# Optimization experiments

Hardware: AMD Instinct MI355X
Metric: run time of the kernel (lower is better)

The kernel has to match this reference:

```python
import jax, jax.numpy as jnp
import numpy as np

B, N, IN_DIM, ATT_DIM = 2, 8192, 512, 512


def setup_inputs() -> dict:
    key = jax.random.key(0)
    k1, k2, k3, k4 = jax.random.split(key, 4)
    X = jax.random.normal(k1, (B, N, IN_DIM), dtype=jnp.float32)
    adj = jax.random.uniform(k2, (B, N, N), dtype=jnp.float32)
    mask = jnp.ones((B, N), dtype=jnp.float32)
    # Learned params (torch Linear stores W as (out,in); we store (in,out) for x @ W)
    Wqk = jax.random.normal(k3, (IN_DIM, 2 * ATT_DIM), dtype=jnp.float32) / np.sqrt(IN_DIM)
    Wv = jax.random.normal(k4, (IN_DIM, IN_DIM), dtype=jnp.float32) / np.sqrt(IN_DIM)
    return {"X": X, "adj": adj, "mask": mask, "Wqk": Wqk, "Wv": Wv}


def reference(X, adj, mask, Wqk, Wv):
    # q, k: (B, N, att_dim); v: (B, N, in_dim)
    qk = X @ Wqk
    q, k = jnp.split(qk, 2, axis=-1)
    v = X @ Wv
    att_dim = q.shape[-1]
    inv_scale = 1.0 / jnp.sqrt(jnp.float32(att_dim))
    # Original math: w_i = inv_scale * sum_j adj_ij * m_i * m_j * (q_i . k_j).
    # Since the rank-1 mask factors (m_i m_j), fold m_j into k and m_i into the row
    # score, avoiding a second materialized NxN tensor:
    k_m = k * mask[:, :, None]                       # (B, N, att_dim)
    agg = jnp.einsum("bij,bjd->bid", adj, k_m)       # (B, N, att_dim)
    w = inv_scale * mask * jnp.einsum("bid,bid->bi", q, agg)  # (B, N)
    # softmax over the bag dimension (dim=1), then scale v rows
    L = jax.nn.softmax(w, axis=1)[:, :, None] * v    # (B, N, in_dim)
    return L
```

## Files before the change

### kernel.cpp

```cpp
#include <hip/hip_runtime.h>
#include <math.h>

#define BB 2
#define NN 8192
#define DD 512

static const float INV_SCALE = 0.04419417382415922f;

typedef short s16x8 __attribute__((ext_vector_type(8)));
typedef unsigned short u16x8 __attribute__((ext_vector_type(8)));
typedef float f32x4 __attribute__((ext_vector_type(4)));

#define AS1 __attribute__((address_space(1)))
#define AS3 __attribute__((address_space(3)))

__device__ __forceinline__ unsigned short bfbits(__bf16 h) {
    return __builtin_bit_cast(unsigned short, h);
}

__device__ __forceinline__ void gll16(const void* g, void* l) {
    __builtin_amdgcn_global_load_lds((const AS1 unsigned int*)g, (AS3 unsigned int*)l, 16, 0, 0);
}

__global__ __launch_bounds__(256) void convx_k(
    const float* __restrict__ X, unsigned short* __restrict__ Xhi,
    unsigned short* __restrict__ Xlo)
{
    long i = (long)blockIdx.x * 256 + threadIdx.x;
    float4 x = ((const float4*)X)[i];
    __bf16 h0 = (__bf16)x.x, h1 = (__bf16)x.y, h2 = (__bf16)x.z, h3 = (__bf16)x.w;
    ushort4 hi4 = make_ushort4(bfbits(h0), bfbits(h1), bfbits(h2), bfbits(h3));
    __bf16 l0 = (__bf16)(x.x - (float)h0), l1 = (__bf16)(x.y - (float)h1);
    __bf16 l2 = (__bf16)(x.z - (float)h2), l3 = (__bf16)(x.w - (float)h3);
    ushort4 lo4 = make_ushort4(bfbits(l0), bfbits(l1), bfbits(l2), bfbits(l3));
    ((ushort4*)Xhi)[i] = hi4;
    ((ushort4*)Xlo)[i] = lo4;
}

__global__ __launch_bounds__(256) void convw_k(
    const float* __restrict__ Wqk, const float* __restrict__ Wv,
    unsigned short* __restrict__ QTh, unsigned short* __restrict__ QTl,
    unsigned short* __restrict__ VTh, unsigned short* __restrict__ VTl)
{
    int i = blockIdx.x * 256 + threadIdx.x;
    float val; unsigned short *ph, *pl;
    if (i < 524288) {
        int n = i >> 9, k = i & 511;
        val = Wqk[k * 1024 + n]; ph = QTh + i; pl = QTl + i;
    } else {
        int o = i - 524288; int n = o >> 9, k = o & 511;
        val = Wv[k * 512 + n]; ph = VTh + o; pl = VTl + o;
    }
    __bf16 h = (__bf16)val;
    __bf16 l = (__bf16)(val - (float)h);
    *ph = bfbits(h); *pl = bfbits(l);
}

template <int EPI, int NT>
__global__ __launch_bounds__(256, 2) void mfma_gemm(
    const unsigned short* __restrict__ A0, const unsigned short* __restrict__ A1,
    const unsigned short* __restrict__ B0, const unsigned short* __restrict__ B1,
    float* __restrict__ C,
    float* __restrict__ q, float* __restrict__ km,
    unsigned short* __restrict__ kmT, const float* __restrict__ mask,
    int N, int K)
{
    constexpr int BK = 32;
    constexpr int TILE_SH = 128 * BK;

    __shared__ unsigned short Asm[2 * TILE_SH];
    __shared__ unsigned short Bsm[2 * TILE_SH];

    const int t = threadIdx.x;
    const int wv = t >> 6, lane = t & 63;
    const int wm = wv >> 1, wn = wv & 1;
    const long m0 = blockIdx.x * 128;
    const int n0 = blockIdx.y * 128;

    f32x4 acc[4][4];
#pragma unroll
    for (int i = 0; i < 4; ++i)
#pragma unroll
        for (int j = 0; j < 4; ++j) acc[i][j] = {0.f, 0.f, 0.f, 0.f};

    const int swzcol = ((lane & 3) ^ ((lane >> 2) & 3)) * 16;
    auto stageA16 = [&](int term, int k0, int buf) {
        const unsigned short* Ab = (term < 2) ? A0 : A1;
#pragma unroll
        for (int u = 0; u < 2; ++u) {
            int c = wv * 2 + u;
            int row = c * 16 + (lane >> 2);
            gll16((const char*)Ab + ((m0 + row) * (long)K + k0) * 2 + swzcol,
                  (char*)Asm + buf * (TILE_SH * 2) + c * 1024);
        }
    };
    auto stageB16 = [&](int term, int k0, int buf) {
        const unsigned short* Bb = (NT == 3 && term == 1) ? B1 : B0;
#pragma unroll
        for (int u = 0; u < 2; ++u) {
            int c = wv * 2 + u;
            int row = c * 16 + (lane >> 2);
            gll16((const char*)Bb + ((long)(n0 + row) * K + k0) * 2 + swzcol,
                  (char*)Bsm + buf * (TILE_SH * 2) + c * 1024);
        }
    };

    stageA16(0, 0, 0);
    stageB16(0, 0, 0);
    __syncthreads();

    const int NTILES = NT * (K / BK);
    int cur = 0, term = 0, k0 = 0;
    const int g = lane >> 4;

#pragma unroll 2
    for (int tt = 0; tt < NTILES; ++tt) {
        int k0n = k0 + BK, termn = term;
        if (k0n == K) { k0n = 0; ++termn; }
        const bool hasNext = (tt + 1 < NTILES);

        if (hasNext) {
            stageA16(termn, k0n, cur ^ 1);
            stageB16(termn, k0n, cur ^ 1);
        }

        s16x8 av[4], bv[4];
#pragma unroll
        for (int f = 0; f < 4; ++f) {
            int ra = wm * 64 + f * 16 + (lane & 15);
            int rb = wn * 64 + f * 16 + (lane & 15);
            av[f] = *(const s16x8*)(Asm + cur * TILE_SH + ra * BK + ((g ^ (ra & 3)) << 3));
            bv[f] = *(const s16x8*)(Bsm + cur * TILE_SH + rb * BK + ((g ^ (rb & 3)) << 3));
        }
#pragma unroll
        for (int fm = 0; fm < 4; ++fm)
#pragma unroll
            for (int fn = 0; fn < 4; ++fn)
                acc[fm][fn] = __builtin_amdgcn_mfma_f32_16x16x32_bf16(
                    av[fm], bv[fn], acc[fm][fn], 0, 0, 0);

        __syncthreads();
        cur ^= 1; term = termn; k0 = k0n;
    }

    const long rbase = m0 + wm * 64;
    const int cbase = n0 + wn * 64;

    if constexpr (EPI == 0) {
#pragma unroll
        for (int fm = 0; fm < 4; ++fm) {
            long rb = rbase + fm * 16 + ((lane >> 4) << 2);
#pragma unroll
            for (int fn = 0; fn < 4; ++fn) {
                int c = cbase + fn * 16 + (lane & 15);
#pragma unroll
                for (int j = 0; j < 4; ++j)
                    C[(rb + j) * (long)N + c] = acc[fm][fn][j];
            }
        }
    } else {
        const bool isq = (n0 < 512);
#pragma unroll
        for (int fm = 0; fm < 4; ++fm) {
            long rb = rbase + fm * 16 + ((lane >> 4) << 2);
#pragma unroll
            for (int fn = 0; fn < 4; ++fn) {
                int c = cbase + fn * 16 + (lane & 15);
                if (isq) {
#pragma unroll
                    for (int j = 0; j < 4; ++j)
                        q[(rb + j) * 512L + c] = acc[fm][fn][j];
                } else {
                    int c2 = c - 512;
                    float kv[4];
#pragma unroll
                    for (int j = 0; j < 4; ++j) {
                        kv[j] = acc[fm][fn][j] * mask[rb + j];
                        km[(rb + j) * 512L + c2] = kv[j];
                    }
                    ushort4 pk = make_ushort4(bfbits((__bf16)kv[0]), bfbits((__bf16)kv[1]),
                                              bfbits((__bf16)kv[2]), bfbits((__bf16)kv[3]));
                    long b = rb >> 13, r = rb & 8191;
                    *(ushort4*)(kmT + (b << 22) + ((long)c2 << 13) + r) = pk;
                }
            }
        }
    }
}

__global__ __launch_bounds__(256, 2) void adj_gemm(
    const float* __restrict__ adj,
    const unsigned short* __restrict__ kmT,
    const float* __restrict__ q,
    float* __restrict__ w)
{
    constexpr int BK = 64;
    constexpr int TS = 128 * BK;
    constexpr int NT = NN / BK;

    __shared__ unsigned short Asm[2 * TS];
    __shared__ unsigned short Bsm[2 * TS];

    const int t = threadIdx.x;
    const int wv = t >> 6, lane = t & 63;
    const int wm = wv >> 1, wn = wv & 1;
    const int z = blockIdx.z;
    const long m0 = blockIdx.x * 128;
    const int n0 = blockIdx.y * 128;

    const float* Az = adj + (long)z * NN * NN;
    const unsigned short* Bz = kmT + ((long)z << 22);

    f32x4 acc[4][4];
#pragma unroll
    for (int i = 0; i < 4; ++i)
#pragma unroll
        for (int j = 0; j < 4; ++j) acc[i][j] = {0.f, 0.f, 0.f, 0.f};

    const int bswz = ((lane & 7) ^ (lane >> 3)) << 4;
    auto stageB = [&](int ttile, int buf) {
        const int k0 = ttile * BK;
#pragma unroll
        for (int u = 0; u < 4; ++u) {
            int c = wv * 4 + u;
            int row = c * 8 + (lane >> 3);
            gll16((const char*)Bz + ((long)(n0 + row) * NN + k0) * 2 + bswz,
                  (char*)Bsm + buf * (TS * 2) + c * 1024);
        }
    };

    const int arow = t >> 1;
    const int asl0 = (t & 1) * 4;
    auto issueA = [&](int ttile, float4 (&r)[8]) {
        const float* s = Az + (m0 + arow) * (long)NN + ttile * BK + asl0 * 8;
#pragma unroll
        for (int u = 0; u < 4; ++u) {
            r[2 * u]     = *(const float4*)(s + u * 8);
            r[2 * u + 1] = *(const float4*)(s + u * 8 + 4);
        }
    };
    auto commitA = [&](float4 (&r)[8], int buf) {
#pragma unroll
        for (int u = 0; u < 4; ++u) {
            float4 a = r[2 * u], b = r[2 * u + 1];
            u16x8 pk;
            pk[0] = bfbits((__bf16)a.x); pk[1] = bfbits((__bf16)a.y);
            pk[2] = bfbits((__bf16)a.z); pk[3] = bfbits((__bf16)a.w);
            pk[4] = bfbits((__bf16)b.x); pk[5] = bfbits((__bf16)b.y);
            pk[6] = bfbits((__bf16)b.z); pk[7] = bfbits((__bf16)b.w);
            *(u16x8*)(Asm + buf * TS + arow * 64 + (((asl0 + u) ^ (arow & 7)) << 3)) = pk;
        }
    };

    const int g = lane >> 4;
    auto compute = [&](int buf) {
#pragma unroll
        for (int ks = 0; ks < 2; ++ks) {
            s16x8 av[4], bv[4];
#pragma unroll
            for (int f = 0; f < 4; ++f) {
                int ra = wm * 64 + f * 16 + (lane & 15);
                int rb = wn * 64 + f * 16 + (lane & 15);
                av[f] = *(const s16x8*)(Asm + buf * TS + ra * 64
                         + (((g + ks * 4) ^ (ra & 7)) << 3));
                bv[f] = *(const s16x8*)(Bsm + buf * TS + rb * 64
                         + (((g + ks * 4) ^ (rb & 7)) << 3));
            }
#pragma unroll
            for (int fm = 0; fm < 4; ++fm)
#pragma unroll
                for (int fn = 0; fn < 4; ++fn)
                    acc[fm][fn] = __builtin_amdgcn_mfma_f32_16x16x32_bf16(
                        av[fm], bv[fn], acc[fm][fn], 0, 0, 0);
        }
    };

#define CBAR() do { \
        asm volatile("s_waitcnt vmcnt(8) lgkmcnt(0)" ::: "memory"); \
        __builtin_amdgcn_s_barrier(); \
        asm volatile("" ::: "memory"); \
    } while (0)

    float4 rA0[8], rA1[8];

    stageB(0, 0);
    __builtin_amdgcn_sched_barrier(0);
    issueA(0, rA0);
    issueA(1, rA1);
    commitA(rA0, 0);
    CBAR();

    for (int tt = 0; tt < NT; tt += 2) {
        if (tt + 1 < NT) stageB(tt + 1, 1);
        __builtin_amdgcn_sched_barrier(0);
        if (tt + 2 < NT) issueA(tt + 2, rA0);
        compute(0);
        if (tt + 1 < NT) commitA(rA1, 1);
        CBAR();
        if (tt + 2 < NT) stageB(tt + 2, 0);
        __builtin_amdgcn_sched_barrier(0);
        if (tt + 3 < NT) issueA(tt + 3, rA1);
        compute(1);
        if (tt + 2 < NT) commitA(rA0, 0);
        CBAR();
    }
#undef CBAR

    const long zrow = (long)z * NN;
    const long rbase = m0 + wm * 64;
    const int cbase = n0 + wn * 64;
#pragma unroll
    for (int fm = 0; fm < 4; ++fm) {
#pragma unroll
        for (int j = 0; j < 4; ++j) {
            long r = zrow + rbase + fm * 16 + ((lane >> 4) << 2) + j;
            const float* qr = q + r * 512L + cbase + (lane & 15);
            float s = 0.f;
#pragma unroll
            for (int fn = 0; fn < 4; ++fn)
                s += qr[fn * 16] * acc[fm][fn][j];
            s += __shfl_xor(s, 1); s += __shfl_xor(s, 2);
            s += __shfl_xor(s, 4); s += __shfl_xor(s, 8);
            if ((lane & 15) == 0) atomicAdd(w + r, s);
        }
    }
}

__global__ __launch_bounds__(256) void fixup_k(
    float* __restrict__ w, const float* __restrict__ mask)
{
    int i = blockIdx.x * 256 + threadIdx.x;
    w[i] *= INV_SCALE * mask[i];
}

__global__ __launch_bounds__(256) void wmax_k(const float* __restrict__ w,
                                              float* __restrict__ wmax)
{
    const int b = blockIdx.x;
    const float* wr = w + (long)b * NN;
    const int t = threadIdx.x;
    float m = -3.4e38f;
    for (int i = t; i < NN; i += 256) m = fmaxf(m, wr[i]);
#pragma unroll
    for (int o = 32; o > 0; o >>= 1) m = fmaxf(m, __shfl_down(m, o));
    __shared__ float red[4];
    if ((t & 63) == 0) red[t >> 6] = m;
    __syncthreads();
    if (t == 0) wmax[b] = fmaxf(fmaxf(red[0], red[1]), fmaxf(red[2], red[3]));
}

__global__ __launch_bounds__(256) void select_k(
    const float* __restrict__ w, const float* __restrict__ wmax,
    int* __restrict__ count, int* __restrict__ cand)
{
    int i = blockIdx.x * 256 + threadIdx.x;
    int b = i >> 13;
    if (w[i] >= wmax[b] - 15.f) {
        int p = atomicAdd(count, 1);
        if (p < 128) cand[p] = i;
    }
}

__global__ __launch_bounds__(256) void refine_k(
    const float* __restrict__ q, const float* __restrict__ km,
    const float* __restrict__ adj, const int* __restrict__ cand,
    const int* __restrict__ count, float* __restrict__ partial)
{
    int y = blockIdx.y;
    int cnt = *count; if (cnt > 128) cnt = 128;
    if (y >= cnt) return;
    const int row = cand[y];
    const int b = row >> 13, r = row & 8191;
    const int x = blockIdx.x;
    const int t = threadIdx.x, w = t >> 6, l = t & 63;

    const float* qr = q + (long)row * 512 + l * 8;
    const float4 q0 = *(const float4*)qr;
    const float4 q1 = *(const float4*)(qr + 4);
    const float* kmB = km + ((long)b << 13) * 512;
    const float* adjR = adj + (((long)b << 13) + r) * 8192L;

    float acc = 0.f;
    const int jbase = x * 128 + w * 32;
    for (int i = 0; i < 32; ++i) {
        int j = jbase + i;
        const float* kr = kmB + (long)j * 512 + l * 8;
        const float4 k0 = *(const float4*)kr;
        const float4 k1 = *(const float4*)(kr + 4);
        float d = q0.x * k0.x + q0.y * k0.y + q0.z * k0.z + q0.w * k0.w
                + q1.x * k1.x + q1.y * k1.y + q1.z * k1.z + q1.w * k1.w;
#pragma unroll
        for (int o = 32; o > 0; o >>= 1) d += __shfl_down(d, o);
        if (l == 0) acc += adjR[j] * d;
    }
    __shared__ float red[4];
    if (l == 0) red[w] = acc;
    __syncthreads();
    if (t == 0) partial[y * 64 + x] = red[0] + red[1] + red[2] + red[3];
}

__global__ __launch_bounds__(128) void apply_k(
    const int* __restrict__ cand, const int* __restrict__ count,
    const float* __restrict__ partial, const float* __restrict__ mask,
    float* __restrict__ w)
{
    int t = threadIdx.x;
    int cnt = *count; if (cnt > 128) cnt = 128;
    if (t < cnt) {
        float s = 0.f;
        for (int x = 0; x < 64; ++x) s += partial[t * 64 + x];
        int row = cand[t];
        w[row] = s * INV_SCALE * mask[row];
    }
}

__global__ __launch_bounds__(1024) void softmax_k(
    const float* __restrict__ w, float* __restrict__ p)
{
    const int b = blockIdx.x;
    const float* wr = w + (long)b * NN;
    float* pr = p + (long)b * NN;
    const int t = threadIdx.x;
    __shared__ float red[16];
    __shared__ float bmax, bsum;

    float m = -3.4e38f;
    for (int i = t; i < NN; i += 1024) m = fmaxf(m, wr[i]);
#pragma unroll
    for (int o = 32; o > 0; o >>= 1) m = fmaxf(m, __shfl_down(m, o));
    if ((t & 63) == 0) red[t >> 6] = m;
    __syncthreads();
    if (t == 0) {
        float mm = red[0];
        for (int i = 1; i < 16; ++i) mm = fmaxf(mm, red[i]);
        bmax = mm;
    }
    __syncthreads();
    const float M = bmax;

    float s = 0.f;
    for (int i = t; i < NN; i += 1024) s += expf(wr[i] - M);
#pragma unroll
    for (int o = 32; o > 0; o >>= 1) s += __shfl_down(s, o);
    __syncthreads();
    if ((t & 63) == 0) red[t >> 6] = s;
    __syncthreads();
    if (t == 0) {
        float ss = 0.f;
        for (int i = 0; i < 16; ++i) ss += red[i];
        bsum = ss;
    }
    __syncthreads();
    const float invS = 1.f / bsum;
    for (int i = t; i < NN; i += 1024) pr[i] = expf(wr[i] - M) * invS;
}

__global__ __launch_bounds__(256) void scale_k(
    const float* __restrict__ v, const float* __restrict__ p,
    float* __restrict__ out)
{
    const long i = (long)blockIdx.x * 256 + threadIdx.x;
    const int row = (int)(i >> 7);
    const float pv = p[row];
    float4 vv = ((const float4*)v)[i];
    vv.x *= pv; vv.y *= pv; vv.z *= pv; vv.w *= pv;
    ((float4*)out)[i] = vv;
}

extern "C" void kernel_launch(void* const* d_in, const int* in_sizes, int n_in,
                              void* d_out, int out_size, void* d_ws, size_t ws_size,
                              hipStream_t stream)
{
    const float* X    = (const float*)d_in[0];
    const float* adj  = (const float*)d_in[1];
    const float* mask = (const float*)d_in[2];
    const float* Wqk  = (const float*)d_in[3];
    const float* Wv   = (const float*)d_in[4];
    float* out = (float*)d_out;

    char* ws = (char*)d_ws;
    const long SZB = 33554432;
    float* q_buf  = (float*)(ws);
    float* km_buf = (float*)(ws + SZB);
    float* v_buf  = (float*)(ws + 2 * SZB);
    unsigned short* Xhi = (unsigned short*)(ws + 3 * SZB);
    unsigned short* Xlo = Xhi + 8388608;
    unsigned short* kmT = (unsigned short*)(ws + 4 * SZB);
    unsigned short* QTh = (unsigned short*)(ws + 4 * SZB + 16777216);
    unsigned short* QTl = QTh + 524288;
    unsigned short* VTh = QTl + 524288;
    unsigned short* VTl = VTh + 262144;
    float* w_buf = (float*)(VTl + 262144);
    float* p_buf = w_buf + 16384;
    float* wmax  = p_buf + 16384;
    float* partial = wmax + 64;
    int* count = (int*)(partial + 8192);
    int* cand  = count + 64;

    hipMemsetAsync(count, 0, 4, stream);
    hipMemsetAsync(w_buf, 0, 16384 * 4, stream);

    convx_k<<<8192, 256, 0, stream>>>(X, Xhi, Xlo);
    convw_k<<<3072, 256, 0, stream>>>(Wqk, Wv, QTh, QTl, VTh, VTl);

    mfma_gemm<1, 3><<<dim3(128, 8, 1), 256, 0, stream>>>(
        Xhi, Xlo, QTh, QTl, nullptr, q_buf, km_buf, kmT, mask, 1024, 512);

    mfma_gemm<0, 1><<<dim3(128, 4, 1), 256, 0, stream>>>(
        Xhi, nullptr, VTh, nullptr, v_buf, nullptr, nullptr, nullptr, nullptr,
        512, 512);

    adj_gemm<<<dim3(64, 4, 2), 256, 0, stream>>>(adj, kmT, q_buf, w_buf);

    fixup_k<<<64, 256, 0, stream>>>(w_buf, mask);

    wmax_k<<<BB, 256, 0, stream>>>(w_buf, wmax);
    select_k<<<64, 256, 0, stream>>>(w_buf, wmax, count, cand);
    refine_k<<<dim3(64, 128, 1), 256, 0, stream>>>(q_buf, km_buf, adj, cand, count, partial);
    apply_k<<<1, 128, 0, stream>>>(cand, count, partial, mask, w_buf);

    softmax_k<<<BB, 1024, 0, stream>>>(w_buf, p_buf);
    scale_k<<<8192, 256, 0, stream>>>(v_buf, p_buf, out);
}
```

Before: 513.5 us.

## Retile adj GEMM to 64-row blocks spanning all 512 columns

```diff
diff --git a/kernel.cpp b/kernel.cpp
--- a/kernel.cpp
+++ b/kernel.cpp
@@ -188,25 +188,23 @@
     }
 }
 
-__global__ __launch_bounds__(256, 2) void adj_gemm(
+__global__ __launch_bounds__(512, 1) void adj_gemm(
     const float* __restrict__ adj,
     const unsigned short* __restrict__ kmT,
     const float* __restrict__ q,
     float* __restrict__ w)
 {
-    constexpr int BK = 64;
-    constexpr int TS = 128 * BK;
-    constexpr int NT = NN / BK;
-
-    __shared__ unsigned short Asm[2 * TS];
-    __shared__ unsigned short Bsm[2 * TS];
+    constexpr int NT = NN / 64;
+    __shared__ unsigned short Asm[2 * 64 * 64];
+    __shared__ unsigned short Bsm[2 * 512 * 64];
 
     const int t = threadIdx.x;
     const int wv = t >> 6, lane = t & 63;
-    const int wm = wv >> 1, wn = wv & 1;
-    const int z = blockIdx.z;
-    const long m0 = blockIdx.x * 128;
-    const int n0 = blockIdx.y * 128;
+
+    const int bid = (int)blockIdx.x;
+    const int lid = (bid & 7) * 32 + (bid >> 3);
+    const int x = lid & 127, z = lid >> 7;
+    const long m0 = (long)x * 64;
 
     const float* Az = adj + (long)z * NN * NN;
     const unsigned short* Bz = kmT + ((long)z << 22);
@@ -218,38 +216,32 @@
         for (int j = 0; j < 4; ++j) acc[i][j] = {0.f, 0.f, 0.f, 0.f};
 
     const int bswz = ((lane & 7) ^ (lane >> 3)) << 4;
-    auto stageB = [&](int ttile, int buf) {
-        const int k0 = ttile * BK;
-#pragma unroll
-        for (int u = 0; u < 4; ++u) {
-            int c = wv * 4 + u;
-            int row = c * 8 + (lane >> 3);
-            gll16((const char*)Bz + ((long)(n0 + row) * NN + k0) * 2 + bswz,
-                  (char*)Bsm + buf * (TS * 2) + c * 1024);
+    auto stageB = [&](int tt, int buf) {
+        const long k0 = (long)tt * 64;
+#pragma unroll
+        for (int u = 0; u < 8; ++u) {
+            int c = wv * 8 + u;
+            int d = c * 8 + (lane >> 3);
+            gll16((const char*)Bz + ((long)d * NN + k0) * 2 + bswz,
+                  (char*)Bsm + buf * 65536 + c * 1024);
         }
     };
 
-    const int arow = t >> 1;
-    const int asl0 = (t & 1) * 4;
-    auto issueA = [&](int ttile, float4 (&r)[8]) {
-        const float* s = Az + (m0 + arow) * (long)NN + ttile * BK + asl0 * 8;
-#pragma unroll
-        for (int u = 0; u < 4; ++u) {
-            r[2 * u]     = *(const float4*)(s + u * 8);
-            r[2 * u + 1] = *(const float4*)(s + u * 8 + 4);
-        }
+    const int arow = t >> 3;
+    const int ac8  = t & 7;
+    auto issueA = [&](int tt, float4 (&r)[2]) {
+        const float* s = Az + (m0 + arow) * (long)NN + (long)tt * 64 + ac8 * 8;
+        r[0] = *(const float4*)s;
+        r[1] = *(const float4*)(s + 4);
     };
-    auto commitA = [&](float4 (&r)[8], int buf) {
-#pragma unroll
-        for (int u = 0; u < 4; ++u) {
-            float4 a = r[2 * u], b = r[2 * u + 1];
-            u16x8 pk;
-            pk[0] = bfbits((__bf16)a.x); pk[1] = bfbits((__bf16)a.y);
-            pk[2] = bfbits((__bf16)a.z); pk[3] = bfbits((__bf16)a.w);
-            pk[4] = bfbits((__bf16)b.x); pk[5] = bfbits((__bf16)b.y);
-            pk[6] = bfbits((__bf16)b.z); pk[7] = bfbits((__bf16)b.w);
-            *(u16x8*)(Asm + buf * TS + arow * 64 + (((asl0 + u) ^ (arow & 7)) << 3)) = pk;
-        }
+    auto commitA = [&](float4 (&r)[2], int buf) {
+        float4 a = r[0], b = r[1];
+        u16x8 pk;
+        pk[0] = bfbits((__bf16)a.x); pk[1] = bfbits((__bf16)a.y);
+        pk[2] = bfbits((__bf16)a.z); pk[3] = bfbits((__bf16)a.w);
+        pk[4] = bfbits((__bf16)b.x); pk[5] = bfbits((__bf16)b.y);
+        pk[6] = bfbits((__bf16)b.z); pk[7] = bfbits((__bf16)b.w);
+        *(u16x8*)(Asm + buf * 4096 + arow * 64 + ((ac8 ^ (arow & 7)) << 3)) = pk;
     };
 
     const int g = lane >> 4;
@@ -259,12 +251,12 @@
             s16x8 av[4], bv[4];
 #pragma unroll
             for (int f = 0; f < 4; ++f) {
-                int ra = wm * 64 + f * 16 + (lane & 15);
-                int rb = wn * 64 + f * 16 + (lane & 15);
-                av[f] = *(const s16x8*)(Asm + buf * TS + ra * 64
-                         + (((g + ks * 4) ^ (ra & 7)) << 3));
-                bv[f] = *(const s16x8*)(Bsm + buf * TS + rb * 64
-                         + (((g + ks * 4) ^ (rb & 7)) << 3));
+                int ma = f * 16 + (lane & 15);
+                int nb = wv * 64 + f * 16 + (lane & 15);
+                av[f] = *(const s16x8*)(Asm + buf * 4096 + ma * 64
+                         + (((g + ks * 4) ^ (ma & 7)) << 3));
+                bv[f] = *(const s16x8*)(Bsm + buf * 32768 + nb * 64
+                         + (((g + ks * 4) ^ (nb & 7)) << 3));
             }
 #pragma unroll
             for (int fm = 0; fm < 4; ++fm)
@@ -275,46 +267,32 @@
         }
     };
 
-#define CBAR() do { \
-        asm volatile("s_waitcnt vmcnt(8) lgkmcnt(0)" ::: "memory"); \
-        __builtin_amdgcn_s_barrier(); \
-        asm volatile("" ::: "memory"); \
-    } while (0)
-
-    float4 rA0[8], rA1[8];
-
+    float4 rA[2];
+    issueA(0, rA);
     stageB(0, 0);
-    __builtin_amdgcn_sched_barrier(0);
-    issueA(0, rA0);
-    issueA(1, rA1);
-    commitA(rA0, 0);
-    CBAR();
-
-    for (int tt = 0; tt < NT; tt += 2) {
-        if (tt + 1 < NT) stageB(tt + 1, 1);
-        __builtin_amdgcn_sched_barrier(0);
-        if (tt + 2 < NT) issueA(tt + 2, rA0);
-        compute(0);
-        if (tt + 1 < NT) commitA(rA1, 1);
-        CBAR();
-        if (tt + 2 < NT) stageB(tt + 2, 0);
-        __builtin_amdgcn_sched_barrier(0);
-        if (tt + 3 < NT) issueA(tt + 3, rA1);
-        compute(1);
-        if (tt + 2 < NT) commitA(rA0, 0);
-        CBAR();
-    }
-#undef CBAR
+    commitA(rA, 0);
+    __syncthreads();
+
+#pragma unroll 2
+    for (int tt = 0; tt < NT; ++tt) {
+        const int cur = tt & 1;
+        const bool hasNext = (tt + 1 < NT);
+        if (hasNext) {
+            issueA(tt + 1, rA);
+            stageB(tt + 1, cur ^ 1);
+        }
+        compute(cur);
+        if (hasNext) commitA(rA, cur ^ 1);
+        __syncthreads();
+    }
 
     const long zrow = (long)z * NN;
-    const long rbase = m0 + wm * 64;
-    const int cbase = n0 + wn * 64;
 #pragma unroll
     for (int fm = 0; fm < 4; ++fm) {
 #pragma unroll
         for (int j = 0; j < 4; ++j) {
-            long r = zrow + rbase + fm * 16 + ((lane >> 4) << 2) + j;
-            const float* qr = q + r * 512L + cbase + (lane & 15);
+            long r = zrow + m0 + fm * 16 + ((lane >> 4) << 2) + j;
+            const float* qr = q + r * 512L + wv * 64 + (lane & 15);
             float s = 0.f;
 #pragma unroll
             for (int fn = 0; fn < 4; ++fn)
@@ -510,7 +488,7 @@
         Xhi, nullptr, VTh, nullptr, v_buf, nullptr, nullptr, nullptr, nullptr,
         512, 512);
 
-    adj_gemm<<<dim3(64, 4, 2), 256, 0, stream>>>(adj, kmT, q_buf, w_buf);
+    adj_gemm<<<256, 512, 0, stream>>>(adj, kmT, q_buf, w_buf);
 
     fixup_k<<<64, 256, 0, stream>>>(w_buf, mask);
 
```

Result: faster. 474.4 us (-7.6%).
